# Optimization experiments

Hardware: AMD Instinct MI355X
Metric: run time of the kernel (lower is better)

The kernel has to match this reference:

```python
import jax, jax.numpy as jnp
import numpy as np
import itertools

CONVEX_K = 10
NUM_CLASS = 100
B, N = 8, 16384
MINDIS_INIT = 1.0e5  # torch code initializes mindis to 100000


def _hull_vertex_labels_np(pts):
    """pts: [G, K, 3] numpy. Exact brute-force 3D convex hull vertex labels
    (general position): a triple is a hull facet iff all points lie on one
    side of its plane; every point on some facet is a hull vertex."""
    G, K, _ = pts.shape
    tri = np.array(list(itertools.combinations(range(K), 3)))  # [T,3]
    a = pts[:, tri[:, 0]]                                      # [G,T,3]
    b = pts[:, tri[:, 1]]
    c = pts[:, tri[:, 2]]
    n = np.cross(b - a, c - a)                                 # [G,T,3]
    d = np.einsum('gkd,gtd->gtk', pts, n) - np.einsum('gtd,gtd->gt', a, n)[:, :, None]
    eps = 1e-7
    facet = (d <= eps).all(-1) | (d >= -eps).all(-1)           # [G,T]
    labels = np.zeros((G, K), dtype=np.int32)
    gidx, tidx = np.nonzero(facet)
    for col in range(3):
        labels[gidx, tri[tidx, col]] = 1
    return labels


def setup_inputs() -> dict:
    key = jax.random.key(0)
    k1, k2, k3 = jax.random.split(key, 3)
    xyz = jax.random.normal(k1, (B, N, 6), dtype=jnp.float32)
    skel_xyz = jax.random.normal(k2, (B, NUM_CLASS * CONVEX_K, 3), dtype=jnp.float32)
    weights = jax.random.normal(k3, (B, NUM_CLASS * CONVEX_K // CONVEX_K * CONVEX_K,), dtype=jnp.float32)[:, :NUM_CLASS * CONVEX_K].reshape(B, -1)[:, :1000]
    weights = jax.random.normal(k3, (B, NUM_CLASS * CONVEX_K), dtype=jnp.float32)
    skel_np = np.asarray(skel_xyz).reshape(B * NUM_CLASS, CONVEX_K, 3)
    labels = jnp.asarray(_hull_vertex_labels_np(skel_np).reshape(B, NUM_CLASS, CONVEX_K))
    return {"xyz": xyz, "skel_xyz": skel_xyz, "weights": weights,
            "labels": labels, "num_class": NUM_CLASS}


def reference(xyz, skel_xyz, weights, labels, num_class):
    b = xyz.shape[0]
    pts = xyz[:, :, :3]                                   # [B,N,3]; normals xyz[:,:,3:6] unused
    cp = skel_xyz.reshape(b, num_class, CONVEX_K, 3)      # [B,C,K,3]

    # --- convex loss: for each non-vertex point, min sq-dist to a hull vertex ---
    diff = cp[:, :, :, None, :] - cp[:, :, None, :, :]    # [B,C,K,K,3] (small)
    sqd = jnp.sum(diff * diff, axis=-1)                   # [B,C,K,K]
    is_vert = labels == 1                                  # [B,C,K]
    masked = jnp.where(is_vert[:, :, None, :], sqd, jnp.inf)
    mindis = jnp.minimum(jnp.min(masked, axis=-1), MINDIS_INIT)  # [B,C,K]
    loss_convex = jnp.sum(jnp.where(is_vert, 0.0, mindis)) / (b * num_class)

    # --- Chamfer (closest_distance_with_batch both directions, L2 norm, summed) ---
    skel = skel_xyz                                        # [B,M,3]
    d2 = (jnp.sum(pts * pts, -1)[:, :, None]
          + jnp.sum(skel * skel, -1)[:, None, :]
          - 2.0 * jnp.einsum('bnd,bmd->bnm', pts, skel))   # [B,N,M]
    d = jnp.sqrt(jnp.maximum(d2, 1e-12))
    loss_cd = (jnp.sum(jnp.min(d, axis=2)) + jnp.sum(jnp.min(d, axis=1))) / b

    return 1.0 * loss_convex + 0.1 * loss_cd
```

## Files before the change

kernel.cpp:

```cpp
#include <hip/hip_runtime.h>

#define BATCH 8
#define NPTS 16384
#define MSKEL 1000
#define NCLS 100
#define CKK 10
#define MINDIS_INITF 100000.0f

#define OFF_PTSM 32000
#define OFF_TMIN (32000 + 524288)
#define OFF_PART (32000 + 524288 + 256000)

__global__ __launch_bounds__(256) void k_prep(const float* __restrict__ xyz,
                                              const float* __restrict__ skel,
                                              float4* __restrict__ skelN,
                                              float4* __restrict__ ptsM,
                                              float* __restrict__ out) {
    const int gid = blockIdx.x * 256 + threadIdx.x;
    {
        const float* p = xyz + (size_t)gid * 6;
        float x = p[0], y = p[1], z = p[2];
        ptsM[gid] = make_float4(x, y, z, 0.5f * (x * x + y * y + z * z));
    }
    if (gid < BATCH * MSKEL) {
        const float* s = skel + (size_t)gid * 3;
        float sx = s[0], sy = s[1], sz = s[2];
        skelN[gid] = make_float4(-sx, -sy, -sz, 0.5f * (sx * sx + sy * sy + sz * sz));
    }
    if (gid == 0) out[0] = 0.0f;
}

__global__ __launch_bounds__(256) void k_chamfer(const float4* __restrict__ skelN,
                                                 const float4* __restrict__ ptsM,
                                                 float* __restrict__ tileMins,
                                                 float* __restrict__ partials) {
    const int bid = blockIdx.x;
    const int tid = threadIdx.x;

    if (bid < 256) {
        const int b = bid >> 5, tile = bid & 31;
        const float4 r0 = ptsM[b * NPTS + tile * 512 + tid];
        const float4 r1 = ptsM[b * NPTS + tile * 512 + 256 + tid];
        const float4* __restrict__ sk = skelN + b * MSKEL;

        float m0A = 3.4e38f, m0B = 3.4e38f, m1A = 3.4e38f, m1B = 3.4e38f;
#pragma unroll 4
        for (int m = 0; m < MSKEL; m += 2) {
            float4 sa = sk[m];
            float4 sb = sk[m + 1];
            float t0a = fmaf(r0.x, sa.x, fmaf(r0.y, sa.y, fmaf(r0.z, sa.z, sa.w)));
            float t1a = fmaf(r1.x, sa.x, fmaf(r1.y, sa.y, fmaf(r1.z, sa.z, sa.w)));
            float t0b = fmaf(r0.x, sb.x, fmaf(r0.y, sb.y, fmaf(r0.z, sb.z, sb.w)));
            float t1b = fmaf(r1.x, sb.x, fmaf(r1.y, sb.y, fmaf(r1.z, sb.z, sb.w)));
            m0A = fminf(m0A, t0a);
            m1A = fminf(m1A, t1a);
            m0B = fminf(m0B, t0b);
            m1B = fminf(m1B, t1b);
        }
        float mt0 = fminf(m0A, m0B), mt1 = fminf(m1A, m1B);
        float d = sqrtf(fmaxf(2.0f * (mt0 + r0.w), 1e-12f)) +
                  sqrtf(fmaxf(2.0f * (mt1 + r1.w), 1e-12f));

#pragma unroll
        for (int o = 32; o > 0; o >>= 1) d += __shfl_down(d, o, 64);
        __shared__ float s_part[4];
        const int wave = tid >> 6, lane = tid & 63;
        if (lane == 0) s_part[wave] = d;
        __syncthreads();
        if (tid == 0) partials[bid] = s_part[0] + s_part[1] + s_part[2] + s_part[3];
    } else {
        const int id = bid - 256;
        const int b = id >> 5, tile = id & 31;

        float nsx[4], nsy[4], nsz[4], ssq[4], mind[4];
#pragma unroll
        for (int k = 0; k < 4; ++k) {
            const int m = tid + k * 256;
            if (m < MSKEL) {
                float4 s = skelN[b * MSKEL + m];
                nsx[k] = s.x; nsy[k] = s.y; nsz[k] = s.z;
                ssq[k] = 2.0f * s.w;
            } else {
                nsx[k] = 0.0f; nsy[k] = 0.0f; nsz[k] = 0.0f; ssq[k] = 0.0f;
            }
            mind[k] = 3.4e38f;
        }

        const float4* __restrict__ pp = ptsM + b * NPTS + tile * 512;
#pragma unroll 8
        for (int n = 0; n < 512; ++n) {
            float4 r = pp[n];
#pragma unroll
            for (int k = 0; k < 4; ++k) {
                float t = fmaf(r.x, nsx[k], fmaf(r.y, nsy[k], fmaf(r.z, nsz[k], r.w)));
                mind[k] = fminf(mind[k], t);
            }
        }
        float* tm = tileMins + (size_t)(b * 32 + tile) * MSKEL;
#pragma unroll
        for (int k = 0; k < 4; ++k) {
            const int m = tid + k * 256;
            if (m < MSKEL) tm[m] = fmaf(2.0f, mind[k], ssq[k]);
        }
    }
}

__global__ __launch_bounds__(256) void k_reduce(const float* __restrict__ skel,
                                                const int* __restrict__ labels,
                                                const float* __restrict__ tileMins,
                                                const float* __restrict__ partials,
                                                float* __restrict__ out) {
    const int gid = blockIdx.x * 256 + threadIdx.x;
    const int tid = threadIdx.x;
    float acc = 0.0f;

    if (gid < BATCH * MSKEL) {
        const int b = gid / MSKEL, m = gid - b * MSKEL;
        float mn = 3.4e38f;
#pragma unroll 8
        for (int t = 0; t < 32; ++t) {
            mn = fminf(mn, tileMins[(size_t)(b * 32 + t) * MSKEL + m]);
        }
        acc += 0.0125f * sqrtf(fmaxf(mn, 1e-12f));
    }
    if (gid < 256) acc += 0.0125f * partials[gid];

    if (gid < BATCH * NCLS) {
        const int b = gid / NCLS, c = gid - b * NCLS;
        const float* cp = skel + ((size_t)b * MSKEL + c * CKK) * 3;
        const int* lab = labels + (size_t)b * NCLS * CKK + c * CKK;
        float x[CKK], y[CKK], z[CKK];
        int lv[CKK];
#pragma unroll
        for (int i = 0; i < CKK; ++i) {
            x[i] = cp[i * 3 + 0]; y[i] = cp[i * 3 + 1]; z[i] = cp[i * 3 + 2];
            lv[i] = lab[i];
        }
        float convexSum = 0.0f;
#pragma unroll
        for (int i = 0; i < CKK; ++i) {
            if (lv[i] != 1) {
                float mind = MINDIS_INITF;
#pragma unroll
                for (int j = 0; j < CKK; ++j) {
                    if (lv[j] == 1) {
                        float dx = x[i] - x[j], dy = y[i] - y[j], dz = z[i] - z[j];
                        mind = fminf(mind, dx * dx + dy * dy + dz * dz);
                    }
                }
                convexSum += mind;
            }
        }
        acc += convexSum * (1.0f / (BATCH * NCLS));
    }

#pragma unroll
    for (int o = 32; o > 0; o >>= 1) acc += __shfl_down(acc, o, 64);
    __shared__ float s_part[4];
    const int wave = tid >> 6, lane = tid & 63;
    if (lane == 0) s_part[wave] = acc;
    __syncthreads();
    if (tid == 0) {
        atomicAdd(out, s_part[0] + s_part[1] + s_part[2] + s_part[3]);
    }
}

extern "C" void kernel_launch(void* const* d_in, const int* in_sizes, int n_in,
                              void* d_out, int out_size, void* d_ws, size_t ws_size,
                              hipStream_t stream) {
    const float* xyz = (const float*)d_in[0];
    const float* skel = (const float*)d_in[1];
    const int* labels = (const int*)d_in[3];
    float* out = (float*)d_out;

    float4* skelN = (float4*)d_ws;
    float4* ptsM = (float4*)((float*)d_ws + OFF_PTSM);
    float* tileMins = (float*)d_ws + OFF_TMIN;
    float* partials = (float*)d_ws + OFF_PART;

    k_prep<<<512, 256, 0, stream>>>(xyz, skel, skelN, ptsM, out);
    k_chamfer<<<512, 256, 0, stream>>>(skelN, ptsM, tileMins, partials);
    k_reduce<<<64, 256, 0, stream>>>(skel, labels, tileMins, partials, out);
}
```

Measured before the change: 104.8 us.

## Split skeleton loop across waves with 8 points per thread; reduce mins via atomics

The points-to-skeleton blocks now give each thread 8 points and each wave a quarter of the skeleton. The per-wave minima are combined in shared memory, which gives more register reuse per skeleton load and shorter serial loops. The skeleton-to-points tile minima are merged with atomicMin on float bits (clamped non-negative) instead of being written to a tileMins buffer, and chamfer partial sums are added atomically to the output. The reduce kernel shrinks to 8 blocks that only read the merged minima. The cost is atomic contention plus an extra shared-memory pass and barrier.

New measurement: 93.10 us. 1.13x faster.

```diff
diff --git a/kernel.cpp b/kernel.cpp
--- a/kernel.cpp
+++ b/kernel.cpp
@@ -8,13 +8,13 @@
 #define MINDIS_INITF 100000.0f
 
 #define OFF_PTSM 32000
-#define OFF_TMIN (32000 + 524288)
-#define OFF_PART (32000 + 524288 + 256000)
+#define OFF_MINB (32000 + 524288)
 
 __global__ __launch_bounds__(256) void k_prep(const float* __restrict__ xyz,
                                               const float* __restrict__ skel,
                                               float4* __restrict__ skelN,
                                               float4* __restrict__ ptsM,
+                                              unsigned int* __restrict__ minbits,
                                               float* __restrict__ out) {
     const int gid = blockIdx.x * 256 + threadIdx.x;
     {
@@ -26,48 +26,63 @@
         const float* s = skel + (size_t)gid * 3;
         float sx = s[0], sy = s[1], sz = s[2];
         skelN[gid] = make_float4(-sx, -sy, -sz, 0.5f * (sx * sx + sy * sy + sz * sz));
+        minbits[gid] = 0x7F800000u;
     }
     if (gid == 0) out[0] = 0.0f;
 }
 
 __global__ __launch_bounds__(256) void k_chamfer(const float4* __restrict__ skelN,
                                                  const float4* __restrict__ ptsM,
-                                                 float* __restrict__ tileMins,
-                                                 float* __restrict__ partials) {
+                                                 unsigned int* __restrict__ minbits,
+                                                 float* __restrict__ out) {
     const int bid = blockIdx.x;
     const int tid = threadIdx.x;
 
     if (bid < 256) {
         const int b = bid >> 5, tile = bid & 31;
-        const float4 r0 = ptsM[b * NPTS + tile * 512 + tid];
-        const float4 r1 = ptsM[b * NPTS + tile * 512 + 256 + tid];
-        const float4* __restrict__ sk = skelN + b * MSKEL;
+        const int wave = tid >> 6, lane = tid & 63;
+        const float4* __restrict__ base = ptsM + b * NPTS + tile * 512;
 
-        float m0A = 3.4e38f, m0B = 3.4e38f, m1A = 3.4e38f, m1B = 3.4e38f;
-#pragma unroll 4
-        for (int m = 0; m < MSKEL; m += 2) {
-            float4 sa = sk[m];
-            float4 sb = sk[m + 1];
-            float t0a = fmaf(r0.x, sa.x, fmaf(r0.y, sa.y, fmaf(r0.z, sa.z, sa.w)));
-            float t1a = fmaf(r1.x, sa.x, fmaf(r1.y, sa.y, fmaf(r1.z, sa.z, sa.w)));
-            float t0b = fmaf(r0.x, sb.x, fmaf(r0.y, sb.y, fmaf(r0.z, sb.z, sb.w)));
-            float t1b = fmaf(r1.x, sb.x, fmaf(r1.y, sb.y, fmaf(r1.z, sb.z, sb.w)));
-            m0A = fminf(m0A, t0a);
-            m1A = fminf(m1A, t1a);
-            m0B = fminf(m0B, t0b);
-            m1B = fminf(m1B, t1b);
+        float4 P[8];
+        float mt[8];
+#pragma unroll
+        for (int j = 0; j < 8; ++j) {
+            P[j] = base[j * 64 + lane];
+            mt[j] = 3.4e38f;
         }
-        float mt0 = fminf(m0A, m0B), mt1 = fminf(m1A, m1B);
-        float d = sqrtf(fmaxf(2.0f * (mt0 + r0.w), 1e-12f)) +
-                  sqrtf(fmaxf(2.0f * (mt1 + r1.w), 1e-12f));
+
+        const float4* __restrict__ sk = skelN + b * MSKEL + wave * 250;
+#pragma unroll 5
+        for (int m = 0; m < 250; ++m) {
+            float4 s = sk[m];
+#pragma unroll
+            for (int j = 0; j < 8; ++j) {
+                float t = fmaf(P[j].x, s.x, fmaf(P[j].y, s.y, fmaf(P[j].z, s.z, s.w)));
+                mt[j] = fminf(mt[j], t);
+            }
+        }
+
+        __shared__ float sm[4 * 512];
+#pragma unroll
+        for (int j = 0; j < 8; ++j) {
+            sm[wave * 512 + j * 64 + lane] = mt[j] + P[j].w;
+        }
+        __syncthreads();
+
+        float a0 = fminf(fminf(sm[tid], sm[512 + tid]),
+                         fminf(sm[1024 + tid], sm[1536 + tid]));
+        float a1 = fminf(fminf(sm[tid + 256], sm[512 + tid + 256]),
+                         fminf(sm[1024 + tid + 256], sm[1536 + tid + 256]));
+        float d = sqrtf(fmaxf(2.0f * a0, 1e-12f)) + sqrtf(fmaxf(2.0f * a1, 1e-12f));
 
 #pragma unroll
         for (int o = 32; o > 0; o >>= 1) d += __shfl_down(d, o, 64);
         __shared__ float s_part[4];
-        const int wave = tid >> 6, lane = tid & 63;
         if (lane == 0) s_part[wave] = d;
         __syncthreads();
-        if (tid == 0) partials[bid] = s_part[0] + s_part[1] + s_part[2] + s_part[3];
+        if (tid == 0) {
+            atomicAdd(out, 0.0125f * (s_part[0] + s_part[1] + s_part[2] + s_part[3]));
+        }
     } else {
         const int id = bid - 256;
         const int b = id >> 5, tile = id & 31;
@@ -96,34 +111,28 @@
                 mind[k] = fminf(mind[k], t);
             }
         }
-        float* tm = tileMins + (size_t)(b * 32 + tile) * MSKEL;
 #pragma unroll
         for (int k = 0; k < 4; ++k) {
             const int m = tid + k * 256;
-            if (m < MSKEL) tm[m] = fmaf(2.0f, mind[k], ssq[k]);
+            if (m < MSKEL) {
+                float d2 = fmaf(2.0f, mind[k], ssq[k]);
+                atomicMin(&minbits[b * MSKEL + m], __float_as_uint(fmaxf(d2, 0.0f)));
+            }
         }
     }
 }
 
 __global__ __launch_bounds__(256) void k_reduce(const float* __restrict__ skel,
                                                 const int* __restrict__ labels,
-                                                const float* __restrict__ tileMins,
-                                                const float* __restrict__ partials,
+                                                const unsigned int* __restrict__ minbits,
                                                 float* __restrict__ out) {
     const int gid = blockIdx.x * 256 + threadIdx.x;
     const int tid = threadIdx.x;
     float acc = 0.0f;
 
-    if (gid < BATCH * MSKEL) {
-        const int b = gid / MSKEL, m = gid - b * MSKEL;
-        float mn = 3.4e38f;
-#pragma unroll 8
-        for (int t = 0; t < 32; ++t) {
-            mn = fminf(mn, tileMins[(size_t)(b * 32 + t) * MSKEL + m]);
-        }
-        acc += 0.0125f * sqrtf(fmaxf(mn, 1e-12f));
+    for (int i = gid; i < BATCH * MSKEL; i += 2048) {
+        acc += 0.0125f * sqrtf(fmaxf(__uint_as_float(minbits[i]), 1e-12f));
     }
-    if (gid < 256) acc += 0.0125f * partials[gid];
 
     if (gid < BATCH * NCLS) {
         const int b = gid / NCLS, c = gid - b * NCLS;
@@ -175,10 +184,9 @@
 
     float4* skelN = (float4*)d_ws;
     float4* ptsM = (float4*)((float*)d_ws + OFF_PTSM);
-    float* tileMins = (float*)d_ws + OFF_TMIN;
-    float* partials = (float*)d_ws + OFF_PART;
+    unsigned int* minbits = (unsigned int*)((float*)d_ws + OFF_MINB);
 
-    k_prep<<<512, 256, 0, stream>>>(xyz, skel, skelN, ptsM, out);
-    k_chamfer<<<512, 256, 0, stream>>>(skelN, ptsM, tileMins, partials);
-    k_reduce<<<64, 256, 0, stream>>>(skel, labels, tileMins, partials, out);
+    k_prep<<<512, 256, 0, stream>>>(xyz, skel, skelN, ptsM, minbits, out);
+    k_chamfer<<<512, 256, 0, stream>>>(skelN, ptsM, minbits, out);
+    k_reduce<<<8, 256, 0, stream>>>(skel, labels, minbits, out);
 }
```
